# Optimization experiments

Hardware: AMD Instinct MI355X
Metric: run time of the kernel (lower is better)

The kernel has to match this reference:

```python
import jax, jax.numpy as jnp
import numpy as np

DIM = 768      # d_model
D_INNER = 768  # int(ssm_ratio * dim)
KK = 16        # K (scan groups)
CD = 48        # Cdim per group (hardcoded self.C)
NS = 16        # d_state
BATCH, SEQ = 8, 4096


def setup_inputs() -> dict:
    key = jax.random.key(0)
    ks = jax.random.split(key, 12)
    s_in = (2.0 / (DIM + 2 * D_INNER)) ** 0.5   # ~xavier
    s_out = (2.0 / (D_INNER + DIM)) ** 0.5
    return {
        "x": jax.random.normal(ks[0], (BATCH, SEQ, DIM), jnp.float32),
        "in_proj_w": jax.random.normal(ks[1], (2 * D_INNER, DIM), jnp.float32) * s_in,
        "in_proj_b": jnp.zeros((2 * D_INNER,), jnp.float32),
        "conv_w": jax.random.normal(ks[2], (D_INNER, 1, 3, 3), jnp.float32) * 0.2,
        "conv_b": jnp.zeros((D_INNER,), jnp.float32),
        "out_proj_w": jax.random.normal(ks[3], (DIM, D_INNER), jnp.float32) * s_out,
        "out_proj_b": jnp.zeros((DIM,), jnp.float32),
        "A_logs": jax.random.normal(ks[4], (KK * CD, NS), jnp.float32) * 0.1,
        "delta": jax.random.normal(ks[5], (BATCH, KK * CD, SEQ), jnp.float32),
        "B_t": jax.random.normal(ks[6], (BATCH, KK, NS, SEQ), jnp.float32),
        "C_t": jax.random.normal(ks[7], (BATCH, KK, NS, SEQ), jnp.float32),
        "delta_bias": jax.random.normal(ks[8], (KK * CD,), jnp.float32),
    }


def reference(x, in_proj_w, in_proj_b, conv_w, conv_b, out_proj_w, out_proj_b,
              A_logs, delta, B_t, C_t, delta_bias):
    # in_proj + chunk; z = silu(z) in the original is dead code (never used)
    h = x @ in_proj_w.T + in_proj_b                      # (B,N,2*D)
    u = h[..., :D_INNER]                                  # (B,N,D)
    # depthwise 3x3 conv on a (B,D,N,1) map (width-1 input, pad 1)
    u = u.transpose(0, 2, 1)[..., None]                   # (B,D,N,1)
    u = jax.lax.conv_general_dilated(
        u, conv_w, window_strides=(1, 1), padding=((1, 1), (1, 1)),
        dimension_numbers=("NCHW", "OIHW", "NCHW"),
        feature_group_count=D_INNER)
    u = jax.nn.silu(u[..., 0] + conv_b[None, :, None])    # (B,D,N)

    # selective_scan_torch math (note: NOT a true recurrence in the source):
    #   delta <- softplus(delta + delta_bias)
    #   y[b,d,l] = delta^2 * u * sum_n A[d,n] * B[b,k(d),n,l] * C[b,k(d),n,l]
    d = jax.nn.softplus(delta + delta_bias[None, :, None])  # (B,D,L)
    A = A_logs.reshape(KK, CD, NS)
    s = jnp.einsum("kcn,bknl->bkcl", A, B_t * C_t)           # (B,K,Cd,L)
    s = s.reshape(u.shape[0], D_INNER, u.shape[2])           # (B,D,L)
    y = d * d * u * s                                        # (B,D,L)

    out = y.transpose(0, 2, 1) @ out_proj_w.T + out_proj_b   # (B,N,dim)
    return out
```

## Files before the change

kernel.cpp:

```cpp
#include <hip/hip_runtime.h>
#include <math.h>

#define B_  8
#define S_  4096
#define D_  768
#define K_  16
#define C_  48
#define N_  16
#define M_  (B_*S_)

typedef float  f32x4  __attribute__((ext_vector_type(4)));
typedef __bf16 bf16x8 __attribute__((ext_vector_type(8)));

__device__ __forceinline__ ushort f2bf(float f) {
  uint u = __builtin_bit_cast(uint, f);
  u += 0x7FFFu + ((u >> 16) & 1u);
  return (ushort)(u >> 16);
}
__device__ __forceinline__ float bf2f(ushort h) {
  return __builtin_bit_cast(float, (uint)h << 16);
}

__global__ __launch_bounds__(256)
void cvt_all(const float* __restrict__ x, const float* __restrict__ w1,
             const float* __restrict__ w2, ushort* __restrict__ xb,
             ushort* __restrict__ wb1, ushort* __restrict__ wb2) {
  const int b = blockIdx.x;
  const float* in; ushort* out; int n4, nb, b0;
  if (b < 2048)      { in = x;  out = xb;  n4 = M_ * D_ / 4; nb = 2048; b0 = 0; }
  else if (b < 2624) { in = w1; out = wb1; n4 = D_ * D_ / 4; nb = 576;  b0 = 2048; }
  else               { in = w2; out = wb2; n4 = D_ * D_ / 4; nb = 576;  b0 = 2624; }
  const int stride = nb * 256;
  for (int i = (b - b0) * 256 + threadIdx.x; i < n4; i += stride) {
    float4 v = *reinterpret_cast<const float4*>(in + (size_t)i * 4);
    ushort4 o;
    o.x = f2bf(v.x); o.y = f2bf(v.y); o.z = f2bf(v.z); o.w = f2bf(v.w);
    *reinterpret_cast<ushort4*>(out + (size_t)i * 4) = o;
  }
}

template<bool OUT_BF16>
__global__ __launch_bounds__(256)
void gemm_mfma_bt(const ushort* __restrict__ A, const ushort* __restrict__ Bm,
                  const float* __restrict__ bias, void* __restrict__ Cc)
{
  __shared__ ushort As[128 * 32];
  __shared__ ushort Bs[128 * 32];

  const int lin = blockIdx.x;
  const int swz = (lin & 7) * 192 + (lin >> 3);
  const int bn  = (swz % 6) * 128;
  const int bm  = (swz / 6) * 128;

  const int tid  = threadIdx.x;
  const int wid  = tid >> 6, lane = tid & 63;
  const int wr   = wid >> 1, wc   = wid & 1;
  const int lr   = lane & 15, lg  = lane >> 4;
  const int srow = lane >> 2;
  const int scol = (lane & 3) * 8;

  f32x4 acc[4][4];
#pragma unroll
  for (int i = 0; i < 4; ++i)
#pragma unroll
    for (int j = 0; j < 4; ++j) acc[i][j] = (f32x4){0.f, 0.f, 0.f, 0.f};

  for (int k0 = 0; k0 < 768; k0 += 32) {
#pragma unroll
    for (int jj = 0; jj < 2; ++jj) {
      const int j = wid * 2 + jj;
      const ushort* ga = A  + (size_t)(bm + j * 16 + srow) * 768 + k0 + scol;
      __builtin_amdgcn_global_load_lds(
          (const __attribute__((address_space(1))) void*)ga,
          (__attribute__((address_space(3))) void*)(As + j * 512), 16, 0, 0);
      const ushort* gb = Bm + (size_t)(bn + j * 16 + srow) * 768 + k0 + scol;
      __builtin_amdgcn_global_load_lds(
          (const __attribute__((address_space(1))) void*)gb,
          (__attribute__((address_space(3))) void*)(Bs + j * 512), 16, 0, 0);
    }
    __syncthreads();

    bf16x8 af[4], bfr[4];
    const int ab = (wr * 64 + lr) * 32 + lg * 8;
    const int bb = (wc * 64 + lr) * 32 + lg * 8;
#pragma unroll
    for (int mf = 0; mf < 4; ++mf) af[mf]  = *reinterpret_cast<const bf16x8*>(&As[ab + mf * 512]);
#pragma unroll
    for (int nf = 0; nf < 4; ++nf) bfr[nf] = *reinterpret_cast<const bf16x8*>(&Bs[bb + nf * 512]);
#pragma unroll
    for (int mf = 0; mf < 4; ++mf)
#pragma unroll
      for (int nf = 0; nf < 4; ++nf)
        acc[mf][nf] = __builtin_amdgcn_mfma_f32_16x16x32_bf16(af[mf], bfr[nf], acc[mf][nf], 0, 0, 0);
    __syncthreads();
  }

#pragma unroll
  for (int nf = 0; nf < 4; ++nf) {
    const int n  = bn + wc * 64 + nf * 16 + lr;
    const float bv = bias[n];
#pragma unroll
    for (int mf = 0; mf < 4; ++mf) {
      const int m0 = bm + wr * 64 + mf * 16 + lg * 4;
#pragma unroll
      for (int r = 0; r < 4; ++r) {
        const float v = acc[mf][nf][r] + bv;
        if (OUT_BF16) ((ushort*)Cc)[(size_t)(m0 + r) * 768 + n] = f2bf(v);
        else          ((float*) Cc)[(size_t)(m0 + r) * 768 + n] = v;
      }
    }
  }
}

#define U0P 67
#define YSP 70

__global__ __launch_bounds__(256)
void fuse_mid(const ushort* __restrict__ u0b, const float* __restrict__ delta,
              const float* __restrict__ Bt, const float* __restrict__ Ct,
              const float* __restrict__ Alog, const float* __restrict__ convw,
              const float* __restrict__ convb, const float* __restrict__ dbias,
              ushort* __restrict__ yT)
{
  __shared__ float  Gs [N_ * 64];
  __shared__ float  Ak [C_ * N_];
  __shared__ ushort U0T[C_ * U0P];
  __shared__ ushort Ys [C_ * YSP];
  __shared__ float  Wk0[C_], Wk1[C_], Wk2[C_], CB[C_], DB[C_];

  const int tid = threadIdx.x;
  const int wid = tid >> 6, lane = tid & 63;
  const int lt = blockIdx.x, k = blockIdx.y, b = blockIdx.z;
  const int l0 = lt * 64;

  for (int idx = tid; idx < N_ * 64; idx += 256) {
    const int n = idx >> 6, dl = idx & 63;
    const size_t gg = (((size_t)b * K_ + k) * N_ + n) * S_ + l0 + dl;
    Gs[idx] = Bt[gg] * Ct[gg];
  }
  for (int idx = tid; idx < C_ * N_; idx += 256)
    Ak[idx] = Alog[(size_t)k * C_ * N_ + idx];
  if (tid < C_) {
    Wk0[tid] = convw[(k * C_ + tid) * 9 + 1];
    Wk1[tid] = convw[(k * C_ + tid) * 9 + 4];
    Wk2[tid] = convw[(k * C_ + tid) * 9 + 7];
    CB [tid] = convb[k * C_ + tid];
    DB [tid] = dbias[k * C_ + tid];
  }
  {
    const uint* usrc = reinterpret_cast<const uint*>(u0b);
    int l = tid / 24, j = tid - (tid / 24) * 24;
    for (int idx = tid; idx < 66 * 24; idx += 256) {
      const int gl = l0 + l - 1;
      uint v = 0;
      if (gl >= 0 && gl < S_) v = usrc[((size_t)b * S_ + gl) * 384 + k * 24 + j];
      U0T[(2 * j    ) * U0P + l] = (ushort)(v & 0xffffu);
      U0T[(2 * j + 1) * U0P + l] = (ushort)(v >> 16);
      l += 10; j += 16; if (j >= 24) { j -= 24; l += 1; }
    }
  }
  __syncthreads();

  float g[N_];
#pragma unroll
  for (int n = 0; n < N_; ++n) g[n] = Gs[n * 64 + lane];

  const float* dp = delta + ((size_t)b * D_ + k * C_ + wid) * S_ + l0 + lane;
  const size_t dstr = (size_t)4 * S_;
  float dn0 = dp[0];
  float dn1 = dp[dstr];

  for (int step = 0; step < 12; ++step) {
    const int c = step * 4 + wid;
    const float dcur = dn0;
    dn0 = dn1;
    dn1 = (step < 10) ? dp[(size_t)(step + 2) * dstr] : 0.f;

    float a[N_];
#pragma unroll
    for (int n4i = 0; n4i < 4; ++n4i)
      *reinterpret_cast<f32x4*>(&a[n4i * 4]) =
          *reinterpret_cast<const f32x4*>(&Ak[c * N_ + n4i * 4]);

    const float dv = dcur + DB[c];
    const float d  = (dv > 15.f) ? dv : __logf(1.f + __expf(dv));

    float xx = fmaf(Wk0[c], bf2f(U0T[c * U0P + lane]),
               fmaf(Wk1[c], bf2f(U0T[c * U0P + lane + 1]),
               fmaf(Wk2[c], bf2f(U0T[c * U0P + lane + 2]), CB[c])));
    const float u = xx * __builtin_amdgcn_rcpf(1.f + __expf(-xx));

    float s = 0.f;
#pragma unroll
    for (int n = 0; n < N_; ++n) s = fmaf(a[n], g[n], s);

    Ys[c * YSP + lane] = f2bf(d * d * u * s);
  }
  __syncthreads();

  {
    int dl = tid / 48, c = tid - (tid / 48) * 48;
    for (int e = tid; e < C_ * 64; e += 256) {
      yT[((size_t)b * S_ + l0 + dl) * D_ + k * C_ + c] = Ys[c * YSP + dl];
      dl += 5; c += 16; if (c >= 48) { c -= 48; dl += 1; }
    }
  }
}

extern "C" void kernel_launch(void* const* d_in, const int* in_sizes, int n_in,
                              void* d_out, int out_size, void* d_ws, size_t ws_size,
                              hipStream_t stream) {
  const float* x      = (const float*)d_in[0];
  const float* in_w   = (const float*)d_in[1];
  const float* in_b   = (const float*)d_in[2];
  const float* convw  = (const float*)d_in[3];
  const float* convb  = (const float*)d_in[4];
  const float* out_w  = (const float*)d_in[5];
  const float* out_b  = (const float*)d_in[6];
  const float* Alog   = (const float*)d_in[7];
  const float* delta  = (const float*)d_in[8];
  const float* Bt     = (const float*)d_in[9];
  const float* Ct     = (const float*)d_in[10];
  const float* dbias  = (const float*)d_in[11];
  float* out = (float*)d_out;

  ushort* xb  = (ushort*)d_ws;
  ushort* u0b = xb  + (size_t)M_ * D_;
  ushort* yTb = u0b + (size_t)M_ * D_;
  ushort* wb1 = yTb + (size_t)M_ * D_;
  ushort* wb2 = wb1 + (size_t)D_ * D_;

  cvt_all<<<3200, 256, 0, stream>>>(x, in_w, out_w, xb, wb1, wb2);

  gemm_mfma_bt<true ><<<1536, 256, 0, stream>>>(xb, wb1, in_b, u0b);
  fuse_mid<<<dim3(S_ / 64, K_, B_), 256, 0, stream>>>(u0b, delta, Bt, Ct, Alog, convw, convb, dbias, yTb);
  gemm_mfma_bt<false><<<1536, 256, 0, stream>>>(yTb, wb2, out_b, out);
}
```

Before: 228.1 us.

## Fuse x bf16 conversion into first GEMM and emit channel-major u0

Drops the separate fp32-to-bf16 pass over x and instead converts x tiles in registers inside the first GEMM before writing them to LDS. That GEMM now writes u0 transposed (channel-major, sequence contiguous), so the mid kernel can read conv neighbours straight from global memory with coalesced loads rather than staging and transposing through LDS. The mid kernel's output store is also packed into 32-bit pairs. The trade-off is that the GEMM's A operand now goes through register loads and LDS stores instead of direct global-to-LDS copies, and the u0 stores are strided by sequence.

New measurement: 259.6 us. 13.8% more time.

```diff
diff --git a/kernel.cpp b/kernel.cpp
--- a/kernel.cpp
+++ b/kernel.cpp
@@ -22,27 +22,203 @@
 }
 
 __global__ __launch_bounds__(256)
-void cvt_all(const float* __restrict__ x, const float* __restrict__ w1,
-             const float* __restrict__ w2, ushort* __restrict__ xb,
-             ushort* __restrict__ wb1, ushort* __restrict__ wb2) {
-  const int b = blockIdx.x;
-  const float* in; ushort* out; int n4, nb, b0;
-  if (b < 2048)      { in = x;  out = xb;  n4 = M_ * D_ / 4; nb = 2048; b0 = 0; }
-  else if (b < 2624) { in = w1; out = wb1; n4 = D_ * D_ / 4; nb = 576;  b0 = 2048; }
-  else               { in = w2; out = wb2; n4 = D_ * D_ / 4; nb = 576;  b0 = 2624; }
-  const int stride = nb * 256;
-  for (int i = (b - b0) * 256 + threadIdx.x; i < n4; i += stride) {
-    float4 v = *reinterpret_cast<const float4*>(in + (size_t)i * 4);
-    ushort4 o;
-    o.x = f2bf(v.x); o.y = f2bf(v.y); o.z = f2bf(v.z); o.w = f2bf(v.w);
-    *reinterpret_cast<ushort4*>(out + (size_t)i * 4) = o;
-  }
-}
-
-template<bool OUT_BF16>
+void cvt_w(const float* __restrict__ w1, const float* __restrict__ w2,
+           ushort* __restrict__ o1, ushort* __restrict__ o2) {
+  const int i = blockIdx.x * 256 + threadIdx.x;
+  const float* src; ushort* dst; int idx;
+  if (i < 147456) { src = w1; dst = o1; idx = i; }
+  else            { src = w2; dst = o2; idx = i - 147456; }
+  float4 v = *reinterpret_cast<const float4*>(src + (size_t)idx * 4);
+  ushort4 o;
+  o.x = f2bf(v.x); o.y = f2bf(v.y); o.z = f2bf(v.z); o.w = f2bf(v.w);
+  *reinterpret_cast<ushort4*>(dst + (size_t)idx * 4) = o;
+}
+
+__global__ __launch_bounds__(256)
+void gemm1_xf32(const float* __restrict__ X, const ushort* __restrict__ Wb,
+                const float* __restrict__ in_b, ushort* __restrict__ u0T)
+{
+  __shared__ ushort As[128 * 32];
+  __shared__ ushort Bs[128 * 32];
+
+  const int lin = blockIdx.x;
+  const int swz = (lin & 7) * 192 + (lin >> 3);
+  const int bn  = (swz % 6) * 128;
+  const int bm  = (swz / 6) * 128;
+
+  const int tid  = threadIdx.x;
+  const int wid  = tid >> 6, lane = tid & 63;
+  const int wr   = wid >> 1, wc   = wid & 1;
+  const int lr   = lane & 15, lg  = lane >> 4;
+  const int srow = lane >> 2;
+  const int scol = (lane & 3) * 8;
+  const int arow = tid >> 2;
+  const int acol = (tid & 3) * 8;
+
+  f32x4 acc[4][4];
+#pragma unroll
+  for (int i = 0; i < 4; ++i)
+#pragma unroll
+    for (int j = 0; j < 4; ++j) acc[i][j] = (f32x4){0.f, 0.f, 0.f, 0.f};
+
+  for (int k0 = 0; k0 < 768; k0 += 32) {
+#pragma unroll
+    for (int half = 0; half < 2; ++half) {
+      const int row = arow + half * 64;
+      const float* xp = X + (size_t)(bm + row) * 768 + k0 + acol;
+      f32x4 v0 = *reinterpret_cast<const f32x4*>(xp);
+      f32x4 v1 = *reinterpret_cast<const f32x4*>(xp + 4);
+      bf16x8 p = {(__bf16)v0[0], (__bf16)v0[1], (__bf16)v0[2], (__bf16)v0[3],
+                  (__bf16)v1[0], (__bf16)v1[1], (__bf16)v1[2], (__bf16)v1[3]};
+      *reinterpret_cast<bf16x8*>(&As[row * 32 + acol]) = p;
+    }
+#pragma unroll
+    for (int jj = 0; jj < 2; ++jj) {
+      const int j = wid * 2 + jj;
+      const ushort* gb = Wb + (size_t)(bn + j * 16 + srow) * 768 + k0 + scol;
+      __builtin_amdgcn_global_load_lds(
+          (const __attribute__((address_space(1))) void*)gb,
+          (__attribute__((address_space(3))) void*)(Bs + j * 512), 16, 0, 0);
+    }
+    __syncthreads();
+
+    bf16x8 af[4], bfr[4];
+    const int ab = (wr * 64 + lr) * 32 + lg * 8;
+    const int bb = (wc * 64 + lr) * 32 + lg * 8;
+#pragma unroll
+    for (int mf = 0; mf < 4; ++mf) af[mf]  = *reinterpret_cast<const bf16x8*>(&As[ab + mf * 512]);
+#pragma unroll
+    for (int nf = 0; nf < 4; ++nf) bfr[nf] = *reinterpret_cast<const bf16x8*>(&Bs[bb + nf * 512]);
+#pragma unroll
+    for (int mf = 0; mf < 4; ++mf)
+#pragma unroll
+      for (int nf = 0; nf < 4; ++nf)
+        acc[mf][nf] = __builtin_amdgcn_mfma_f32_16x16x32_bf16(af[mf], bfr[nf], acc[mf][nf], 0, 0, 0);
+    __syncthreads();
+  }
+
+  const int b   = bm >> 12;
+  const int l0g = (bm & 4095) + wr * 64;
+#pragma unroll
+  for (int nf = 0; nf < 4; ++nf) {
+    const int cg = bn + wc * 64 + nf * 16 + lr;
+    const float bv = in_b[cg];
+    ushort* up = u0T + ((size_t)b * 768 + cg) * 4096 + l0g;
+#pragma unroll
+    for (int mf = 0; mf < 4; ++mf) {
+      ushort4 o;
+      o.x = f2bf(acc[mf][nf][0] + bv);
+      o.y = f2bf(acc[mf][nf][1] + bv);
+      o.z = f2bf(acc[mf][nf][2] + bv);
+      o.w = f2bf(acc[mf][nf][3] + bv);
+      *reinterpret_cast<ushort4*>(up + mf * 16 + lg * 4) = o;
+    }
+  }
+}
+
+#define YSP 70
+
+__global__ __launch_bounds__(256)
+void fuse_mid(const ushort* __restrict__ u0T, const float* __restrict__ delta,
+              const float* __restrict__ Bt, const float* __restrict__ Ct,
+              const float* __restrict__ Alog, const float* __restrict__ convw,
+              const float* __restrict__ convb, const float* __restrict__ dbias,
+              ushort* __restrict__ yT)
+{
+  __shared__ float  Gs [N_ * 64];
+  __shared__ float  Ak [C_ * N_];
+  __shared__ ushort Ys [C_ * YSP];
+  __shared__ float  Wk0[C_], Wk1[C_], Wk2[C_], CB[C_], DB[C_];
+
+  const int tid = threadIdx.x;
+  const int wid = tid >> 6, lane = tid & 63;
+  const int lt = blockIdx.x, k = blockIdx.y, b = blockIdx.z;
+  const int l0 = lt * 64;
+
+  for (int idx = tid; idx < N_ * 64; idx += 256) {
+    const int n = idx >> 6, dl = idx & 63;
+    const size_t gg = (((size_t)b * K_ + k) * N_ + n) * S_ + l0 + dl;
+    Gs[idx] = Bt[gg] * Ct[gg];
+  }
+  for (int idx = tid; idx < C_ * N_; idx += 256)
+    Ak[idx] = Alog[(size_t)k * C_ * N_ + idx];
+  if (tid < C_) {
+    Wk0[tid] = convw[(k * C_ + tid) * 9 + 1];
+    Wk1[tid] = convw[(k * C_ + tid) * 9 + 4];
+    Wk2[tid] = convw[(k * C_ + tid) * 9 + 7];
+    CB [tid] = convb[k * C_ + tid];
+    DB [tid] = dbias[k * C_ + tid];
+  }
+  __syncthreads();
+
+  float g[N_];
+#pragma unroll
+  for (int n = 0; n < N_; ++n) g[n] = Gs[n * 64 + lane];
+
+  const int  gl    = l0 + lane;
+  const bool lm_ok = gl > 0;
+  const bool lp_ok = gl < (S_ - 1);
+  const size_t base = ((size_t)b * D_ + k * C_ + wid) * S_ + gl;
+  const float*  dp = delta + base;
+  const ushort* up = u0T + base;
+  const size_t cs = (size_t)4 * S_;
+
+  float dA = dp[0];
+  float umA = lm_ok ? bf2f(up[-1]) : 0.f;
+  float u0A = bf2f(up[0]);
+  float upA = lp_ok ? bf2f(up[1]) : 0.f;
+  float dB = dp[cs];
+  float umB = lm_ok ? bf2f(up[cs - 1]) : 0.f;
+  float u0B = bf2f(up[cs]);
+  float upB = lp_ok ? bf2f(up[cs + 1]) : 0.f;
+
+  for (int step = 0; step < 12; ++step) {
+    const int c = step * 4 + wid;
+    const float dcur = dA, um = umA, u0v = u0A, upv = upA;
+    dA = dB; umA = umB; u0A = u0B; upA = upB;
+    if (step < 10) {
+      const size_t off = (size_t)(step + 2) * cs;
+      dB  = dp[off];
+      umB = lm_ok ? bf2f(up[off - 1]) : 0.f;
+      u0B = bf2f(up[off]);
+      upB = lp_ok ? bf2f(up[off + 1]) : 0.f;
+    }
+
+    float a[N_];
+#pragma unroll
+    for (int n4i = 0; n4i < 4; ++n4i)
+      *reinterpret_cast<f32x4*>(&a[n4i * 4]) =
+          *reinterpret_cast<const f32x4*>(&Ak[c * N_ + n4i * 4]);
+
+    const float dv = dcur + DB[c];
+    const float d  = (dv > 15.f) ? dv : __logf(1.f + __expf(dv));
+
+    float xx = fmaf(Wk0[c], um, fmaf(Wk1[c], u0v, fmaf(Wk2[c], upv, CB[c])));
+    const float u = xx * __builtin_amdgcn_rcpf(1.f + __expf(-xx));
+
+    float s = 0.f;
+#pragma unroll
+    for (int n = 0; n < N_; ++n) s = fmaf(a[n], g[n], s);
+
+    Ys[c * YSP + lane] = f2bf(d * d * u * s);
+  }
+  __syncthreads();
+
+  {
+    uint* yTu = reinterpret_cast<uint*>(yT);
+    int dl = tid / 24, j = tid - (tid / 24) * 24;
+    for (int e = tid; e < 64 * 24; e += 256) {
+      const uint lo = Ys[(2 * j    ) * YSP + dl];
+      const uint hi = Ys[(2 * j + 1) * YSP + dl];
+      yTu[((size_t)b * S_ + l0 + dl) * 384 + k * 24 + j] = lo | (hi << 16);
+      dl += 10; j += 16; if (j >= 24) { j -= 24; dl += 1; }
+    }
+  }
+}
+
 __global__ __launch_bounds__(256)
 void gemm_mfma_bt(const ushort* __restrict__ A, const ushort* __restrict__ Bm,
-                  const float* __restrict__ bias, void* __restrict__ Cc)
+                  const float* __restrict__ bias, float* __restrict__ Cc)
 {
   __shared__ ushort As[128 * 32];
   __shared__ ushort Bs[128 * 32];
@@ -103,106 +279,8 @@
     for (int mf = 0; mf < 4; ++mf) {
       const int m0 = bm + wr * 64 + mf * 16 + lg * 4;
 #pragma unroll
-      for (int r = 0; r < 4; ++r) {
-        const float v = acc[mf][nf][r] + bv;
-        if (OUT_BF16) ((ushort*)Cc)[(size_t)(m0 + r) * 768 + n] = f2bf(v);
-        else          ((float*) Cc)[(size_t)(m0 + r) * 768 + n] = v;
-      }
-    }
-  }
-}
-
-#define U0P 67
-#define YSP 70
-
-__global__ __launch_bounds__(256)
-void fuse_mid(const ushort* __restrict__ u0b, const float* __restrict__ delta,
-              const float* __restrict__ Bt, const float* __restrict__ Ct,
-              const float* __restrict__ Alog, const float* __restrict__ convw,
-              const float* __restrict__ convb, const float* __restrict__ dbias,
-              ushort* __restrict__ yT)
-{
-  __shared__ float  Gs [N_ * 64];
-  __shared__ float  Ak [C_ * N_];
-  __shared__ ushort U0T[C_ * U0P];
-  __shared__ ushort Ys [C_ * YSP];
-  __shared__ float  Wk0[C_], Wk1[C_], Wk2[C_], CB[C_], DB[C_];
-
-  const int tid = threadIdx.x;
-  const int wid = tid >> 6, lane = tid & 63;
-  const int lt = blockIdx.x, k = blockIdx.y, b = blockIdx.z;
-  const int l0 = lt * 64;
-
-  for (int idx = tid; idx < N_ * 64; idx += 256) {
-    const int n = idx >> 6, dl = idx & 63;
-    const size_t gg = (((size_t)b * K_ + k) * N_ + n) * S_ + l0 + dl;
-    Gs[idx] = Bt[gg] * Ct[gg];
-  }
-  for (int idx = tid; idx < C_ * N_; idx += 256)
-    Ak[idx] = Alog[(size_t)k * C_ * N_ + idx];
-  if (tid < C_) {
-    Wk0[tid] = convw[(k * C_ + tid) * 9 + 1];
-    Wk1[tid] = convw[(k * C_ + tid) * 9 + 4];
-    Wk2[tid] = convw[(k * C_ + tid) * 9 + 7];
-    CB [tid] = convb[k * C_ + tid];
-    DB [tid] = dbias[k * C_ + tid];
-  }
-  {
-    const uint* usrc = reinterpret_cast<const uint*>(u0b);
-    int l = tid / 24, j = tid - (tid / 24) * 24;
-    for (int idx = tid; idx < 66 * 24; idx += 256) {
-      const int gl = l0 + l - 1;
-      uint v = 0;
-      if (gl >= 0 && gl < S_) v = usrc[((size_t)b * S_ + gl) * 384 + k * 24 + j];
-      U0T[(2 * j    ) * U0P + l] = (ushort)(v & 0xffffu);
-      U0T[(2 * j + 1) * U0P + l] = (ushort)(v >> 16);
-      l += 10; j += 16; if (j >= 24) { j -= 24; l += 1; }
-    }
-  }
-  __syncthreads();
-
-  float g[N_];
-#pragma unroll
-  for (int n = 0; n < N_; ++n) g[n] = Gs[n * 64 + lane];
-
-  const float* dp = delta + ((size_t)b * D_ + k * C_ + wid) * S_ + l0 + lane;
-  const size_t dstr = (size_t)4 * S_;
-  float dn0 = dp[0];
-  float dn1 = dp[dstr];
-
-  for (int step = 0; step < 12; ++step) {
-    const int c = step * 4 + wid;
-    const float dcur = dn0;
-    dn0 = dn1;
-    dn1 = (step < 10) ? dp[(size_t)(step + 2) * dstr] : 0.f;
-
-    float a[N_];
-#pragma unroll
-    for (int n4i = 0; n4i < 4; ++n4i)
-      *reinterpret_cast<f32x4*>(&a[n4i * 4]) =
-          *reinterpret_cast<const f32x4*>(&Ak[c * N_ + n4i * 4]);
-
-    const float dv = dcur + DB[c];
-    const float d  = (dv > 15.f) ? dv : __logf(1.f + __expf(dv));
-
-    float xx = fmaf(Wk0[c], bf2f(U0T[c * U0P + lane]),
-               fmaf(Wk1[c], bf2f(U0T[c * U0P + lane + 1]),
-               fmaf(Wk2[c], bf2f(U0T[c * U0P + lane + 2]), CB[c])));
-    const float u = xx * __builtin_amdgcn_rcpf(1.f + __expf(-xx));
-
-    float s = 0.f;
-#pragma unroll
-    for (int n = 0; n < N_; ++n) s = fmaf(a[n], g[n], s);
-
-    Ys[c * YSP + lane] = f2bf(d * d * u * s);
-  }
-  __syncthreads();
-
-  {
-    int dl = tid / 48, c = tid - (tid / 48) * 48;
-    for (int e = tid; e < C_ * 64; e += 256) {
-      yT[((size_t)b * S_ + l0 + dl) * D_ + k * C_ + c] = Ys[c * YSP + dl];
-      dl += 5; c += 16; if (c >= 48) { c -= 48; dl += 1; }
+      for (int r = 0; r < 4; ++r)
+        Cc[(size_t)(m0 + r) * 768 + n] = acc[mf][nf][r] + bv;
     }
   }
 }
@@ -224,15 +302,14 @@
   const float* dbias  = (const float*)d_in[11];
   float* out = (float*)d_out;
 
-  ushort* xb  = (ushort*)d_ws;
-  ushort* u0b = xb  + (size_t)M_ * D_;
-  ushort* yTb = u0b + (size_t)M_ * D_;
+  ushort* u0T = (ushort*)d_ws;
+  ushort* yTb = u0T + (size_t)M_ * D_;
   ushort* wb1 = yTb + (size_t)M_ * D_;
   ushort* wb2 = wb1 + (size_t)D_ * D_;
 
-  cvt_all<<<3200, 256, 0, stream>>>(x, in_w, out_w, xb, wb1, wb2);
-
-  gemm_mfma_bt<true ><<<1536, 256, 0, stream>>>(xb, wb1, in_b, u0b);
-  fuse_mid<<<dim3(S_ / 64, K_, B_), 256, 0, stream>>>(u0b, delta, Bt, Ct, Alog, convw, convb, dbias, yTb);
-  gemm_mfma_bt<false><<<1536, 256, 0, stream>>>(yTb, wb2, out_b, out);
-}
+  cvt_w<<<1152, 256, 0, stream>>>(in_w, out_w, wb1, wb2);
+  gemm1_xf32<<<1536, 256, 0, stream>>>(x, wb1, in_b, u0T);
+  fuse_mid<<<dim3(S_ / 64, K_, B_), 256, 0, stream>>>(u0T, delta, Bt, Ct, Alog,
+                                                      convw, convb, dbias, yTb);
+  gemm_mfma_bt<<<1536, 256, 0, stream>>>(yTb, wb2, out_b, out);
+}
```
